# Performance work log

Measured on AMD Instinct MI355X. Metric: run time of the kernel, lower is better.

## Reference

```python
import jax, jax.numpy as jnp
import numpy as np

EPS = 1e-12  # matches torch F.normalize default eps


def setup_inputs() -> dict:
    key = jax.random.key(0)
    img_feats = jax.random.normal(key, (8192, 1024), dtype=jnp.float32)
    return {"img_feats": img_feats}


def reference(img_feats):
    # L2-normalize along feature dim (torch F.normalize: x / max(||x||, eps))
    norm = jnp.maximum(jnp.linalg.norm(img_feats, axis=-1, keepdims=True), EPS)
    feats_n = img_feats / norm                       # [N, D]
    sims = feats_n @ feats_n.T                        # [N, N] cosine similarities
    # mask self-similarity on the diagonal with -inf
    n = sims.shape[0]
    diag = jnp.arange(n)
    sims = sims.at[diag, diag].set(-jnp.inf)
    attn_weights = jax.nn.softmax(sims, axis=-1)      # [N, N]
    out = attn_weights @ img_feats                    # [N, D]
    return out, attn_weights
```

## Files before the change

kernel.cpp:

```cpp
#include <hip/hip_runtime.h>
#include <hip/hip_bf16.h>
#include <stdint.h>

#define NR 8192
#define ND 1024

typedef __attribute__((ext_vector_type(8))) short bf16x8;
typedef __attribute__((ext_vector_type(4))) float f32x4;
typedef __attribute__((ext_vector_type(4))) float fvec4;
typedef __attribute__((ext_vector_type(8))) unsigned short u16x8;

static __device__ __forceinline__ uint16_t f2bf(float f) {
  union { __hip_bfloat16 h; uint16_t u; } cv;
  cv.h = __float2bfloat16(f);
  return cv.u;
}
static __device__ __forceinline__ float bf2f(uint16_t u) {
  union { uint32_t i; float f; } cv;
  cv.i = ((uint32_t)u) << 16;
  return cv.f;
}

__global__ void k_norm(const float* __restrict__ X, uint16_t* __restrict__ Xn) {
  const int row = blockIdx.x;
  const int t = threadIdx.x;
  const float4 v = reinterpret_cast<const float4*>(X + (size_t)row * ND)[t];
  float ss = v.x * v.x + v.y * v.y + v.z * v.z + v.w * v.w;
#pragma unroll
  for (int m = 1; m < 64; m <<= 1) ss += __shfl_xor(ss, m, 64);
  __shared__ float sred[4];
  if ((t & 63) == 0) sred[t >> 6] = ss;
  __syncthreads();
  const float tot = sred[0] + sred[1] + sred[2] + sred[3];
  const float inv = 1.0f / fmaxf(sqrtf(tot), 1e-12f);
  ushort4 o;
  o.x = f2bf(v.x * inv); o.y = f2bf(v.y * inv);
  o.z = f2bf(v.z * inv); o.w = f2bf(v.w * inv);
  reinterpret_cast<ushort4*>(Xn + (size_t)row * ND)[t] = o;
}

__global__ void k_transpose(const float* __restrict__ X, uint16_t* __restrict__ XT) {
  __shared__ uint16_t tile[32][33];
  const int ntr = NR / 32;
  const int bx = blockIdx.x % ntr;
  const int by = blockIdx.x / ntr;
  const int r0 = bx * 32, d0 = by * 32;
  const int t = threadIdx.x;
  const int rr = t >> 3, cc = (t & 7) * 4;
  const float4 v = *reinterpret_cast<const float4*>(&X[(size_t)(r0 + rr) * ND + d0 + cc]);
  tile[cc + 0][rr] = f2bf(v.x);
  tile[cc + 1][rr] = f2bf(v.y);
  tile[cc + 2][rr] = f2bf(v.z);
  tile[cc + 3][rr] = f2bf(v.w);
  __syncthreads();
  ushort4 o;
  o.x = tile[rr][cc + 0]; o.y = tile[rr][cc + 1];
  o.z = tile[rr][cc + 2]; o.w = tile[rr][cc + 3];
  *reinterpret_cast<ushort4*>(&XT[(size_t)(d0 + rr) * NR + r0 + cc]) = o;
}

template <int MH, int NH>
static __device__ __forceinline__ void mfma16(f32x4 (&acc)[8][4],
                                              const bf16x8 (&a_)[4][2],
                                              const bf16x8 (&b_)[2][2]) {
  __builtin_amdgcn_s_setprio(1);
#pragma unroll
  for (int kk = 0; kk < 2; ++kk)
#pragma unroll
    for (int m4 = 0; m4 < 4; ++m4)
#pragma unroll
      for (int n2 = 0; n2 < 2; ++n2)
        acc[MH * 4 + m4][NH * 2 + n2] = __builtin_amdgcn_mfma_f32_16x16x32_bf16(
            a_[m4][kk], b_[n2][kk], acc[MH * 4 + m4][NH * 2 + n2], 0, 0, 0);
  __builtin_amdgcn_s_setprio(0);
}

#define BAR()    __builtin_amdgcn_s_barrier()
#define LGKM()   asm volatile("s_waitcnt lgkmcnt(0)" ::: "memory")
#define VMW4()   asm volatile("s_waitcnt vmcnt(4)" ::: "memory")
#define VMW0()   asm volatile("s_waitcnt vmcnt(0)" ::: "memory")
#define SCHED0() __builtin_amdgcn_sched_barrier(0)

template <int EPI, int NKT>
static __device__ __forceinline__ void gemm8_core(
    char* sm,
    const uint16_t* __restrict__ A, int lda,
    const uint16_t* __restrict__ B, int ldb,
    int row0, int col0,
    float* __restrict__ C, int ldc,
    uint16_t* __restrict__ Eo, float* __restrict__ partials, int rb, int cb,
    float* __restrict__ emitA, const float* __restrict__ invrs, int bx_emit) {
  const int tid = threadIdx.x;
  const int wid = tid >> 6;
  const int lane = tid & 63;
  const int wr = wid >> 2;
  const int wc = wid & 3;
  const int flane = lane & 15;
  const int qw = lane >> 4;
  const int rkey = flane & 7;
  const int rowb = flane * 128;

  const int colb = (((tid & 7) ^ ((tid >> 3) & 7)) * 16);
  const int r0s = tid >> 3;

  const char* const Abyte = (const char*)A + (size_t)row0 * lda * 2;
  const char* const Bbyte = (const char*)B + (size_t)col0 * ldb * 2;

  f32x4 acc[8][4] = {};
  bf16x8 a_[4][2], b_[2][2];

  float invr0 = 0, invr1 = 0, invr2 = 0, invr3 = 0;
  if constexpr (EPI == 1) {
    const int rb0 = tid >> 3;
    invr0 = invrs[row0 + rb0];
    invr1 = invrs[row0 + 64 + rb0];
    invr2 = invrs[row0 + 128 + rb0];
    invr3 = invrs[row0 + 192 + rb0];
  }

  auto stageH = [&](int d, int isB, int h, int t) {
    const char* gb = isB ? Bbyte : Abyte;
    const int ld2 = (isB ? ldb : lda) * 2;
    const char* g0 = gb + (size_t)(h * 128 + r0s) * ld2 + t * 128 + colb;
    const char* g1 = g0 + (size_t)64 * ld2;
    char* l0 = sm + d * 65536 + isB * 32768 + h * 16384 + (wid << 10);
    __builtin_amdgcn_global_load_lds((const __attribute__((address_space(1))) void*)g0,
                                     (__attribute__((address_space(3))) void*)l0, 16, 0, 0);
    __builtin_amdgcn_global_load_lds((const __attribute__((address_space(1))) void*)g1,
                                     (__attribute__((address_space(3))) void*)(l0 + 8192), 16, 0, 0);
  };
  auto rdA = [&](int d, int mhalf) {
#pragma unroll
    for (int m4 = 0; m4 < 4; ++m4)
#pragma unroll
      for (int kk = 0; kk < 2; ++kk) {
        const int chunk = (qw + kk * 4) ^ rkey;
        a_[m4][kk] = *(const bf16x8*)(sm + d * 65536 + wr * 16384 +
                                      (mhalf * 4 + m4) * 2048 + rowb + chunk * 16);
      }
  };
  auto rdB = [&](int d, int nhalf) {
#pragma unroll
    for (int n2 = 0; n2 < 2; ++n2)
#pragma unroll
      for (int kk = 0; kk < 2; ++kk) {
        const int chunk = (qw + kk * 4) ^ rkey;
        b_[n2][kk] = *(const bf16x8*)(sm + d * 65536 + 32768 + (wc >> 1) * 16384 +
                                      (wc & 1) * 8192 + (nhalf * 2 + n2) * 2048 +
                                      rowb + chunk * 16);
      }
  };
  auto emitT = [&](int d, int t) {
    const int c8 = tid & 7;
    const int rbase = tid >> 3;
#pragma unroll
    for (int p = 0; p < 4; ++p) {
      const int r = p * 64 + rbase;
      const u16x8 ev = *(const u16x8*)(sm + d * 65536 + ((r >> 7) * 16384) +
                                       (r & 127) * 128 + ((c8 ^ (r & 7)) << 4));
      const float inv = (p == 0) ? invr0 : (p == 1) ? invr1 : (p == 2) ? invr2 : invr3;
      fvec4 o0, o1;
      o0.x = bf2f(ev[0]) * inv; o0.y = bf2f(ev[1]) * inv;
      o0.z = bf2f(ev[2]) * inv; o0.w = bf2f(ev[3]) * inv;
      o1.x = bf2f(ev[4]) * inv; o1.y = bf2f(ev[5]) * inv;
      o1.z = bf2f(ev[6]) * inv; o1.w = bf2f(ev[7]) * inv;
      float* dst = emitA + (size_t)(row0 + r) * NR + t * 64 + c8 * 8;
      __builtin_nontemporal_store(o0, (fvec4*)dst);
      __builtin_nontemporal_store(o1, (fvec4*)(dst + 4));
    }
  };

  stageH(0, 0, 0, 0); stageH(0, 0, 1, 0); stageH(0, 1, 0, 0); stageH(0, 1, 1, 0);
  stageH(1, 0, 0, 1); stageH(1, 0, 1, 1);
  VMW4();
  BAR();

  const int niter = NKT / 2;
  for (int i = 0; i < niter; ++i) {
    const int t0 = 2 * i, t1 = t0 + 1;
    const bool s0 = (t0 + 2 < NKT), s1 = (t1 + 2 < NKT);
    const bool doEmit = (EPI == 1) && ((t0 >> 4) == bx_emit);
    rdA(0, 0); rdB(0, 0);
    stageH(1, 1, 0, t1); stageH(1, 1, 1, t1);
    BAR(); LGKM(); SCHED0(); mfma16<0, 0>(acc, a_, b_); BAR();
    rdB(0, 1);
    BAR(); LGKM(); SCHED0(); mfma16<0, 1>(acc, a_, b_); BAR();
    rdA(0, 1);
    BAR(); LGKM(); SCHED0(); mfma16<1, 1>(acc, a_, b_); BAR();
    if constexpr (EPI == 1) {
      if (doEmit) { emitT(0, t0); LGKM(); BAR(); }
    }
    rdB(0, 0);
    if (s0) { stageH(0, 0, 0, t0 + 2); stageH(0, 0, 1, t0 + 2); }
    BAR(); LGKM(); SCHED0(); mfma16<1, 0>(acc, a_, b_);
    if (s0) { VMW4(); } else { VMW0(); }
    BAR();
    rdA(1, 0); rdB(1, 0);
    if (s0) { stageH(0, 1, 0, t0 + 2); stageH(0, 1, 1, t0 + 2); }
    BAR(); LGKM(); SCHED0(); mfma16<0, 0>(acc, a_, b_); BAR();
    rdB(1, 1);
    BAR(); LGKM(); SCHED0(); mfma16<0, 1>(acc, a_, b_); BAR();
    rdA(1, 1);
    BAR(); LGKM(); SCHED0(); mfma16<1, 1>(acc, a_, b_); BAR();
    if constexpr (EPI == 1) {
      if (doEmit) { emitT(1, t1); LGKM(); BAR(); }
    }
    rdB(1, 0);
    if (s1) { stageH(1, 0, 0, t1 + 2); stageH(1, 0, 1, t1 + 2); }
    BAR(); LGKM(); SCHED0(); mfma16<1, 0>(acc, a_, b_);
    if (s1) { VMW4(); } else if (s0) { VMW0(); }
    BAR();
  }

  const int e0 = (lane >> 4) * 4;

  if constexpr (EPI == 0) {
    const bool diag = (rb == cb);
    float rp[8][4] = {};
    float rpT[4] = {};
#pragma unroll
    for (int m = 0; m < 8; ++m) {
      const int growb = row0 + wr * 128 + m * 16 + e0;
#pragma unroll
      for (int n = 0; n < 4; ++n) {
        const int gcol = col0 + wc * 64 + n * 16 + flane;
        ushort4 mpack;
#pragma unroll
        for (int e = 0; e < 4; ++e) {
          const int grow = growb + e;
          const float ev = (grow == gcol) ? 0.0f : __expf(acc[m][n][e]);
          const uint16_t eb = f2bf(ev);
          const float evr = bf2f(eb);
          Eo[(size_t)grow * NR + gcol] = eb;
          rp[m][e] += evr;
          rpT[n] += evr;
          ((uint16_t*)&mpack)[e] = eb;
        }
        if (!diag) {
          const int mr = wc * 64 + n * 16 + flane;
          const int mc = wr * 128 + m * 16 + e0;
          int byte = mr * 512 + mc * 2;
          byte ^= (mr & 7) << 4;
          *reinterpret_cast<ushort4*>(sm + byte) = mpack;
        }
      }
    }
#pragma unroll
    for (int msk = 1; msk <= 8; msk <<= 1)
#pragma unroll
      for (int m = 0; m < 8; ++m)
#pragma unroll
        for (int e = 0; e < 4; ++e) rp[m][e] += __shfl_xor(rp[m][e], msk, 64);
#pragma unroll
    for (int msk = 16; msk <= 32; msk <<= 1)
#pragma unroll
      for (int n = 0; n < 4; ++n) rpT[n] += __shfl_xor(rpT[n], msk, 64);

    __syncthreads();
    if (!diag) {
#pragma unroll
      for (int p = 0; p < 16; ++p) {
        const int mr = p * 16 + (tid >> 5);
        const int ch = tid & 31;
        int byte = mr * 512 + ch * 16;
        byte ^= (mr & 7) << 4;
        const u16x8 v = *reinterpret_cast<const u16x8*>(sm + byte);
        *reinterpret_cast<u16x8*>(&Eo[(size_t)(col0 + mr) * NR + row0 + ch * 8]) = v;
      }
    }
    __syncthreads();

    float* sRow = (float*)sm;
    float* sCol = (float*)(sm + 4096);
    if (flane == 0) {
#pragma unroll
      for (int m = 0; m < 8; ++m)
#pragma unroll
        for (int e = 0; e < 4; ++e)
          sRow[wc * 256 + wr * 128 + m * 16 + e0 + e] = rp[m][e];
    }
    if (lane < 16) {
#pragma unroll
      for (int n = 0; n < 4; ++n) sCol[wr * 256 + wc * 64 + n * 16 + lane] = rpT[n];
    }
    __syncthreads();
    if (tid < 256) {
      partials[(size_t)cb * NR + row0 + tid] =
          sRow[tid] + sRow[256 + tid] + sRow[512 + tid] + sRow[768 + tid];
      if (!diag)
        partials[(size_t)rb * NR + col0 + tid] = sCol[tid] + sCol[256 + tid];
    }
  } else {
#pragma unroll
    for (int m = 0; m < 8; ++m)
#pragma unroll
      for (int n = 0; n < 4; ++n)
#pragma unroll
        for (int e = 0; e < 4; ++e)
          C[(size_t)(row0 + wr * 128 + m * 16 + e0 + e) * ldc +
            col0 + wc * 64 + n * 16 + flane] = acc[m][n][e];
  }
}

__global__ __launch_bounds__(512, 2) void k_gemm_sym8(
    const uint16_t* __restrict__ Xn, uint16_t* __restrict__ E,
    float* __restrict__ partials) {
  extern __shared__ char smem[];
  const int nwg = gridDim.x;
  const int cpx = nwg >> 3;
  const int b = blockIdx.x;
  const int swz = (b & 7) * cpx + (b >> 3);
  int rem = swz, rb = 0;
  while (rem >= 32 - rb) { rem -= 32 - rb; ++rb; }
  const int cb = rb + rem;
  gemm8_core<0, 16>(smem, Xn, ND, Xn, ND, rb * 256, cb * 256,
                    nullptr, 0, E, partials, rb, cb, nullptr, nullptr, -1);
}

__global__ __launch_bounds__(512, 2) void k_gemm_pv8(
    const uint16_t* __restrict__ E, const uint16_t* __restrict__ XT,
    float* __restrict__ P, float* __restrict__ attn,
    const float* __restrict__ invrs) {
  extern __shared__ char smem[];
  const int b = blockIdx.x;
  const int swz = (b & 7) * 32 + (b >> 3);
  const int s = swz >> 7;
  const int t = swz & 127;
  const int by = t >> 2, bx = t & 3;
  gemm8_core<1, 64>(smem, E + (size_t)s * 4096, NR, XT + (size_t)s * 4096, NR,
                    by * 256, bx * 256, P + (size_t)s * NR * ND, ND,
                    nullptr, nullptr, 0, 0,
                    attn + (size_t)s * 4096, invrs, bx);
}

__global__ void k_rowsum(const float* __restrict__ partials, float* __restrict__ rowsum,
                         int ncb) {
  const int r = blockIdx.x * blockDim.x + threadIdx.x;
  float s = 0.0f;
  for (int cb = 0; cb < ncb; ++cb) s += partials[(size_t)cb * NR + r];
  rowsum[r] = 1.0f / s;
}

__global__ void k_fixup(const fvec4* __restrict__ P0, const fvec4* __restrict__ P1,
                        const float* __restrict__ rowsum, fvec4* __restrict__ out) {
  const size_t i = (size_t)blockIdx.x * blockDim.x + threadIdx.x;
  const int row = (int)(i >> 8);
  const float inv = rowsum[row];
  const fvec4 a = __builtin_nontemporal_load(&P0[i]);
  const fvec4 b = __builtin_nontemporal_load(&P1[i]);
  const fvec4 o = (a + b) * inv;
  __builtin_nontemporal_store(o, &out[i]);
}

extern "C" void kernel_launch(void* const* d_in, const int* in_sizes, int n_in,
                              void* d_out, int out_size, void* d_ws, size_t ws_size,
                              hipStream_t stream) {
  const float* X = (const float*)d_in[0];
  float* out = (float*)d_out;
  float* attn = out + (size_t)NR * ND;

  char* ws = (char*)d_ws;
  const size_t off_Xn   = 0;
  const size_t off_XT   = off_Xn + (size_t)NR * ND * 2;
  const size_t off_E    = off_XT + (size_t)ND * NR * 2;
  const size_t off_part = off_E + (size_t)NR * NR * 2;
  const size_t off_rs   = off_part + (size_t)64 * NR * 4;
  const size_t off_P    = off_rs + (size_t)NR * 4;
  const size_t needed   = off_P + (size_t)2 * NR * ND * 4;
  if (ws_size < needed) return;

  uint16_t* Xn  = (uint16_t*)(ws + off_Xn);
  uint16_t* XT  = (uint16_t*)(ws + off_XT);
  uint16_t* E   = (uint16_t*)(ws + off_E);
  float* partials = (float*)(ws + off_part);
  float* rowsum   = (float*)(ws + off_rs);
  float* P        = (float*)(ws + off_P);

  (void)hipFuncSetAttribute((const void*)k_gemm_sym8,
                            hipFuncAttributeMaxDynamicSharedMemorySize, 131072);
  (void)hipFuncSetAttribute((const void*)k_gemm_pv8,
                            hipFuncAttributeMaxDynamicSharedMemorySize, 131072);

  k_norm<<<NR, 256, 0, stream>>>(X, Xn);
  k_transpose<<<(NR / 32) * (ND / 32), 256, 0, stream>>>(X, XT);
  k_gemm_sym8<<<528, 512, 131072, stream>>>(Xn, E, partials);
  k_rowsum<<<NR / 256, 256, 0, stream>>>(partials, rowsum, 32);
  k_gemm_pv8<<<256, 512, 131072, stream>>>(E, XT, P, attn, rowsum);
  k_fixup<<<NR * ND / 4 / 256, 256, 0, stream>>>(
      (const fvec4*)P, (const fvec4*)(P + (size_t)NR * ND), rowsum, (fvec4*)out);
}
```

Before: 303.6 us.

## Rewrite PV GEMM with K=32 tiles and a four-stage load pipeline

```diff
diff --git a/kernel.cpp b/kernel.cpp
--- a/kernel.cpp
+++ b/kernel.cpp
@@ -9,6 +9,9 @@
 typedef __attribute__((ext_vector_type(4))) float f32x4;
 typedef __attribute__((ext_vector_type(4))) float fvec4;
 typedef __attribute__((ext_vector_type(8))) unsigned short u16x8;
+
+#define AS1 __attribute__((address_space(1)))
+#define AS3 __attribute__((address_space(3)))
 
 static __device__ __forceinline__ uint16_t f2bf(float f) {
   union { __hip_bfloat16 h; uint16_t u; } cv;
@@ -77,19 +80,16 @@
 
 #define BAR()    __builtin_amdgcn_s_barrier()
 #define LGKM()   asm volatile("s_waitcnt lgkmcnt(0)" ::: "memory")
+#define VMW12()  asm volatile("s_waitcnt vmcnt(12)" ::: "memory")
+#define VMW8()   asm volatile("s_waitcnt vmcnt(8)" ::: "memory")
 #define VMW4()   asm volatile("s_waitcnt vmcnt(4)" ::: "memory")
 #define VMW0()   asm volatile("s_waitcnt vmcnt(0)" ::: "memory")
 #define SCHED0() __builtin_amdgcn_sched_barrier(0)
 
-template <int EPI, int NKT>
-static __device__ __forceinline__ void gemm8_core(
-    char* sm,
-    const uint16_t* __restrict__ A, int lda,
-    const uint16_t* __restrict__ B, int ldb,
-    int row0, int col0,
-    float* __restrict__ C, int ldc,
-    uint16_t* __restrict__ Eo, float* __restrict__ partials, int rb, int cb,
-    float* __restrict__ emitA, const float* __restrict__ invrs, int bx_emit) {
+template <int NKT>
+static __device__ __forceinline__ void gemm_sym_core(
+    char* sm, const uint16_t* __restrict__ A, int lda, int row0, int col0,
+    uint16_t* __restrict__ Eo, float* __restrict__ partials, int rb, int cb) {
   const int tid = threadIdx.x;
   const int wid = tid >> 6;
   const int lane = tid & 63;
@@ -104,30 +104,19 @@
   const int r0s = tid >> 3;
 
   const char* const Abyte = (const char*)A + (size_t)row0 * lda * 2;
-  const char* const Bbyte = (const char*)B + (size_t)col0 * ldb * 2;
+  const char* const Bbyte = (const char*)A + (size_t)col0 * lda * 2;
 
   f32x4 acc[8][4] = {};
   bf16x8 a_[4][2], b_[2][2];
 
-  float invr0 = 0, invr1 = 0, invr2 = 0, invr3 = 0;
-  if constexpr (EPI == 1) {
-    const int rb0 = tid >> 3;
-    invr0 = invrs[row0 + rb0];
-    invr1 = invrs[row0 + 64 + rb0];
-    invr2 = invrs[row0 + 128 + rb0];
-    invr3 = invrs[row0 + 192 + rb0];
-  }
-
   auto stageH = [&](int d, int isB, int h, int t) {
     const char* gb = isB ? Bbyte : Abyte;
-    const int ld2 = (isB ? ldb : lda) * 2;
+    const int ld2 = lda * 2;
     const char* g0 = gb + (size_t)(h * 128 + r0s) * ld2 + t * 128 + colb;
     const char* g1 = g0 + (size_t)64 * ld2;
     char* l0 = sm + d * 65536 + isB * 32768 + h * 16384 + (wid << 10);
-    __builtin_amdgcn_global_load_lds((const __attribute__((address_space(1))) void*)g0,
-                                     (__attribute__((address_space(3))) void*)l0, 16, 0, 0);
-    __builtin_amdgcn_global_load_lds((const __attribute__((address_space(1))) void*)g1,
-                                     (__attribute__((address_space(3))) void*)(l0 + 8192), 16, 0, 0);
+    __builtin_amdgcn_global_load_lds((const AS1 void*)g0, (AS3 void*)l0, 16, 0, 0);
+    __builtin_amdgcn_global_load_lds((const AS1 void*)g1, (AS3 void*)(l0 + 8192), 16, 0, 0);
   };
   auto rdA = [&](int d, int mhalf) {
 #pragma unroll
@@ -150,25 +139,6 @@
                                       rowb + chunk * 16);
       }
   };
-  auto emitT = [&](int d, int t) {
-    const int c8 = tid & 7;
-    const int rbase = tid >> 3;
-#pragma unroll
-    for (int p = 0; p < 4; ++p) {
-      const int r = p * 64 + rbase;
-      const u16x8 ev = *(const u16x8*)(sm + d * 65536 + ((r >> 7) * 16384) +
-                                       (r & 127) * 128 + ((c8 ^ (r & 7)) << 4));
-      const float inv = (p == 0) ? invr0 : (p == 1) ? invr1 : (p == 2) ? invr2 : invr3;
-      fvec4 o0, o1;
-      o0.x = bf2f(ev[0]) * inv; o0.y = bf2f(ev[1]) * inv;
-      o0.z = bf2f(ev[2]) * inv; o0.w = bf2f(ev[3]) * inv;
-      o1.x = bf2f(ev[4]) * inv; o1.y = bf2f(ev[5]) * inv;
-      o1.z = bf2f(ev[6]) * inv; o1.w = bf2f(ev[7]) * inv;
-      float* dst = emitA + (size_t)(row0 + r) * NR + t * 64 + c8 * 8;
-      __builtin_nontemporal_store(o0, (fvec4*)dst);
-      __builtin_nontemporal_store(o1, (fvec4*)(dst + 4));
-    }
-  };
 
   stageH(0, 0, 0, 0); stageH(0, 0, 1, 0); stageH(0, 1, 0, 0); stageH(0, 1, 1, 0);
   stageH(1, 0, 0, 1); stageH(1, 0, 1, 1);
@@ -179,7 +149,6 @@
   for (int i = 0; i < niter; ++i) {
     const int t0 = 2 * i, t1 = t0 + 1;
     const bool s0 = (t0 + 2 < NKT), s1 = (t1 + 2 < NKT);
-    const bool doEmit = (EPI == 1) && ((t0 >> 4) == bx_emit);
     rdA(0, 0); rdB(0, 0);
     stageH(1, 1, 0, t1); stageH(1, 1, 1, t1);
     BAR(); LGKM(); SCHED0(); mfma16<0, 0>(acc, a_, b_); BAR();
@@ -187,9 +156,6 @@
     BAR(); LGKM(); SCHED0(); mfma16<0, 1>(acc, a_, b_); BAR();
     rdA(0, 1);
     BAR(); LGKM(); SCHED0(); mfma16<1, 1>(acc, a_, b_); BAR();
-    if constexpr (EPI == 1) {
-      if (doEmit) { emitT(0, t0); LGKM(); BAR(); }
-    }
     rdB(0, 0);
     if (s0) { stageH(0, 0, 0, t0 + 2); stageH(0, 0, 1, t0 + 2); }
     BAR(); LGKM(); SCHED0(); mfma16<1, 0>(acc, a_, b_);
@@ -202,9 +168,6 @@
     BAR(); LGKM(); SCHED0(); mfma16<0, 1>(acc, a_, b_); BAR();
     rdA(1, 1);
     BAR(); LGKM(); SCHED0(); mfma16<1, 1>(acc, a_, b_); BAR();
-    if constexpr (EPI == 1) {
-      if (doEmit) { emitT(1, t1); LGKM(); BAR(); }
-    }
     rdB(1, 0);
     if (s1) { stageH(1, 0, 0, t1 + 2); stageH(1, 0, 1, t1 + 2); }
     BAR(); LGKM(); SCHED0(); mfma16<1, 0>(acc, a_, b_);
@@ -213,92 +176,80 @@
   }
 
   const int e0 = (lane >> 4) * 4;
-
-  if constexpr (EPI == 0) {
-    const bool diag = (rb == cb);
-    float rp[8][4] = {};
-    float rpT[4] = {};
-#pragma unroll
-    for (int m = 0; m < 8; ++m) {
-      const int growb = row0 + wr * 128 + m * 16 + e0;
-#pragma unroll
-      for (int n = 0; n < 4; ++n) {
-        const int gcol = col0 + wc * 64 + n * 16 + flane;
-        ushort4 mpack;
-#pragma unroll
-        for (int e = 0; e < 4; ++e) {
-          const int grow = growb + e;
-          const float ev = (grow == gcol) ? 0.0f : __expf(acc[m][n][e]);
-          const uint16_t eb = f2bf(ev);
-          const float evr = bf2f(eb);
-          Eo[(size_t)grow * NR + gcol] = eb;
-          rp[m][e] += evr;
-          rpT[n] += evr;
-          ((uint16_t*)&mpack)[e] = eb;
-        }
-        if (!diag) {
-          const int mr = wc * 64 + n * 16 + flane;
-          const int mc = wr * 128 + m * 16 + e0;
-          int byte = mr * 512 + mc * 2;
-          byte ^= (mr & 7) << 4;
-          *reinterpret_cast<ushort4*>(sm + byte) = mpack;
-        }
+  const bool diag = (rb == cb);
+  float rp[8][4] = {};
+  float rpT[4] = {};
+#pragma unroll
+  for (int m = 0; m < 8; ++m) {
+    const int growb = row0 + wr * 128 + m * 16 + e0;
+#pragma unroll
+    for (int n = 0; n < 4; ++n) {
+      const int gcol = col0 + wc * 64 + n * 16 + flane;
+      ushort4 mpack;
+#pragma unroll
+      for (int e = 0; e < 4; ++e) {
+        const int grow = growb + e;
+        const float ev = (grow == gcol) ? 0.0f : __expf(acc[m][n][e]);
+        const uint16_t eb = f2bf(ev);
+        const float evr = bf2f(eb);
+        Eo[(size_t)grow * NR + gcol] = eb;
+        rp[m][e] += evr;
+        rpT[n] += evr;
+        ((uint16_t*)&mpack)[e] = eb;
+      }
+      if (!diag) {
+        const int mr = wc * 64 + n * 16 + flane;
+        const int mc = wr * 128 + m * 16 + e0;
+        int byte = mr * 512 + mc * 2;
+        byte ^= (mr & 7) << 4;
+        *reinterpret_cast<ushort4*>(sm + byte) = mpack;
       }
     }
-#pragma unroll
-    for (int msk = 1; msk <= 8; msk <<= 1)
-#pragma unroll
-      for (int m = 0; m < 8; ++m)
-#pragma unroll
-        for (int e = 0; e < 4; ++e) rp[m][e] += __shfl_xor(rp[m][e], msk, 64);
-#pragma unroll
-    for (int msk = 16; msk <= 32; msk <<= 1)
-#pragma unroll
-      for (int n = 0; n < 4; ++n) rpT[n] += __shfl_xor(rpT[n], msk, 64);
-
-    __syncthreads();
-    if (!diag) {
-#pragma unroll
-      for (int p = 0; p < 16; ++p) {
-        const int mr = p * 16 + (tid >> 5);
-        const int ch = tid & 31;
-        int byte = mr * 512 + ch * 16;
-        byte ^= (mr & 7) << 4;
-        const u16x8 v = *reinterpret_cast<const u16x8*>(sm + byte);
-        *reinterpret_cast<u16x8*>(&Eo[(size_t)(col0 + mr) * NR + row0 + ch * 8]) = v;
-      }
+  }
+#pragma unroll
+  for (int msk = 1; msk <= 8; msk <<= 1)
+#pragma unroll
+    for (int m = 0; m < 8; ++m)
+#pragma unroll
+      for (int e = 0; e < 4; ++e) rp[m][e] += __shfl_xor(rp[m][e], msk, 64);
+#pragma unroll
+  for (int msk = 16; msk <= 32; msk <<= 1)
+#pragma unroll
+    for (int n = 0; n < 4; ++n) rpT[n] += __shfl_xor(rpT[n], msk, 64);
+
+  __syncthreads();
+  if (!diag) {
+#pragma unroll
+    for (int p = 0; p < 16; ++p) {
+      const int mr = p * 16 + (tid >> 5);
+      const int ch = tid & 31;
+      int byte = mr * 512 + ch * 16;
+      byte ^= (mr & 7) << 4;
+      const u16x8 v = *reinterpret_cast<const u16x8*>(sm + byte);
+      *reinterpret_cast<u16x8*>(&Eo[(size_t)(col0 + mr) * NR + row0 + ch * 8]) = v;
     }
-    __syncthreads();
-
-    float* sRow = (float*)sm;
-    float* sCol = (float*)(sm + 4096);
-    if (flane == 0) {
-#pragma unroll
-      for (int m = 0; m < 8; ++m)
-#pragma unroll
-        for (int e = 0; e < 4; ++e)
-          sRow[wc * 256 + wr * 128 + m * 16 + e0 + e] = rp[m][e];
-    }
-    if (lane < 16) {
-#pragma unroll
-      for (int n = 0; n < 4; ++n) sCol[wr * 256 + wc * 64 + n * 16 + lane] = rpT[n];
-    }
-    __syncthreads();
-    if (tid < 256) {
-      partials[(size_t)cb * NR + row0 + tid] =
-          sRow[tid] + sRow[256 + tid] + sRow[512 + tid] + sRow[768 + tid];
-      if (!diag)
-        partials[(size_t)rb * NR + col0 + tid] = sCol[tid] + sCol[256 + tid];
-    }
-  } else {
+  }
+  __syncthreads();
+
+  float* sRow = (float*)sm;
+  float* sCol = (float*)(sm + 4096);
+  if (flane == 0) {
 #pragma unroll
     for (int m = 0; m < 8; ++m)
 #pragma unroll
-      for (int n = 0; n < 4; ++n)
-#pragma unroll
-        for (int e = 0; e < 4; ++e)
-          C[(size_t)(row0 + wr * 128 + m * 16 + e0 + e) * ldc +
-            col0 + wc * 64 + n * 16 + flane] = acc[m][n][e];
+      for (int e = 0; e < 4; ++e)
+        sRow[wc * 256 + wr * 128 + m * 16 + e0 + e] = rp[m][e];
+  }
+  if (lane < 16) {
+#pragma unroll
+    for (int n = 0; n < 4; ++n) sCol[wr * 256 + wc * 64 + n * 16 + lane] = rpT[n];
+  }
+  __syncthreads();
+  if (tid < 256) {
+    partials[(size_t)cb * NR + row0 + tid] =
+        sRow[tid] + sRow[256 + tid] + sRow[512 + tid] + sRow[768 + tid];
+    if (!diag)
+      partials[(size_t)rb * NR + col0 + tid] = sCol[tid] + sCol[256 + tid];
   }
 }
 
@@ -313,11 +264,10 @@
   int rem = swz, rb = 0;
   while (rem >= 32 - rb) { rem -= 32 - rb; ++rb; }
   const int cb = rb + rem;
-  gemm8_core<0, 16>(smem, Xn, ND, Xn, ND, rb * 256, cb * 256,
-                    nullptr, 0, E, partials, rb, cb, nullptr, nullptr, -1);
-}
-
-__global__ __launch_bounds__(512, 2) void k_gemm_pv8(
+  gemm_sym_core<16>(smem, Xn, ND, rb * 256, cb * 256, E, partials, rb, cb);
+}
+
+__global__ __launch_bounds__(512, 2) void k_pv32(
     const uint16_t* __restrict__ E, const uint16_t* __restrict__ XT,
     float* __restrict__ P, float* __restrict__ attn,
     const float* __restrict__ invrs) {
@@ -325,12 +275,106 @@
   const int b = blockIdx.x;
   const int swz = (b & 7) * 32 + (b >> 3);
   const int s = swz >> 7;
-  const int t = swz & 127;
-  const int by = t >> 2, bx = t & 3;
-  gemm8_core<1, 64>(smem, E + (size_t)s * 4096, NR, XT + (size_t)s * 4096, NR,
-                    by * 256, bx * 256, P + (size_t)s * NR * ND, ND,
-                    nullptr, nullptr, 0, 0,
-                    attn + (size_t)s * 4096, invrs, bx);
+  const int t4 = swz & 127;
+  const int by = t4 >> 2, bx = t4 & 3;
+  const int row0 = by * 256, col0 = bx * 256;
+
+  const int tid = threadIdx.x;
+  const int wid = tid >> 6;
+  const int lane = tid & 63;
+  const int wr = wid >> 2;
+  const int wc = wid & 3;
+  const int flane = lane & 15;
+  const int qw = lane >> 4;
+  const int keyL = (flane & 3) ^ ((flane >> 2) & 3);
+
+  const int skey = ((tid >> 2) & 3) ^ ((tid >> 4) & 3);
+  const int scol = ((tid & 3) ^ skey) << 4;
+  const int srow = tid >> 2;
+
+  const char* const Abyte = (const char*)(E + (size_t)s * 4096) + (size_t)row0 * NR * 2;
+  const char* const Bbyte = (const char*)(XT + (size_t)s * 4096) + (size_t)col0 * NR * 2;
+  float* const Pp = P + (size_t)s * NR * ND;
+  float* const emitA = attn + (size_t)s * 4096;
+
+  f32x4 acc[8][4] = {};
+
+  const float invr = invrs[row0 + (tid >> 1)];
+  const int keyE = ((tid >> 1) & 3) ^ ((tid >> 3) & 3);
+
+  auto stage = [&](int d, int t) {
+#pragma unroll
+    for (int isB = 0; isB < 2; ++isB)
+#pragma unroll
+      for (int h = 0; h < 2; ++h) {
+        const char* g = (isB ? Bbyte : Abyte) +
+                        (size_t)(h * 128 + srow) * (NR * 2) + t * 64 + scol;
+        char* l = smem + d * 32768 + isB * 16384 + h * 8192 + (wid << 10);
+        __builtin_amdgcn_global_load_lds((const AS1 void*)g, (AS3 void*)l, 16, 0, 0);
+      }
+  };
+
+  auto compute = [&](int d, int t, bool doEmit) {
+    bf16x8 a_[8], b_[4];
+#pragma unroll
+    for (int m = 0; m < 8; ++m) {
+      const int row = wr * 128 + m * 16 + flane;
+      a_[m] = *(const bf16x8*)(smem + d * 32768 + row * 64 + ((qw ^ keyL) << 4));
+    }
+#pragma unroll
+    for (int n = 0; n < 4; ++n) {
+      const int row = wc * 64 + n * 16 + flane;
+      b_[n] = *(const bf16x8*)(smem + d * 32768 + 16384 + row * 64 + ((qw ^ keyL) << 4));
+    }
+    LGKM(); SCHED0();
+    __builtin_amdgcn_s_setprio(1);
+#pragma unroll
+    for (int m = 0; m < 8; ++m)
+#pragma unroll
+      for (int n = 0; n < 4; ++n)
+        acc[m][n] = __builtin_amdgcn_mfma_f32_16x16x32_bf16(a_[m], b_[n], acc[m][n], 0, 0, 0);
+    __builtin_amdgcn_s_setprio(0);
+    if (doEmit) {
+      const int r = tid >> 1;
+#pragma unroll
+      for (int j = 0; j < 2; ++j) {
+        const int c = (tid & 1) * 2 + j;
+        const u16x8 ev = *(const u16x8*)(smem + d * 32768 + r * 64 + ((c ^ keyE) << 4));
+        fvec4 o0, o1;
+        o0.x = bf2f(ev[0]) * invr; o0.y = bf2f(ev[1]) * invr;
+        o0.z = bf2f(ev[2]) * invr; o0.w = bf2f(ev[3]) * invr;
+        o1.x = bf2f(ev[4]) * invr; o1.y = bf2f(ev[5]) * invr;
+        o1.z = bf2f(ev[6]) * invr; o1.w = bf2f(ev[7]) * invr;
+        float* dst = emitA + (size_t)(row0 + r) * NR + t * 32 + c * 8;
+        __builtin_nontemporal_store(o0, (fvec4*)dst);
+        __builtin_nontemporal_store(o1, (fvec4*)(dst + 4));
+      }
+      LGKM();
+    }
+  };
+
+  constexpr int NKT = 128;
+  stage(0, 0); stage(1, 1); stage(2, 2);
+  for (int t = 0; t < NKT - 3; ++t) {
+    stage((t + 3) & 3, t + 3);
+    VMW12();
+    BAR();
+    compute(t & 3, t, (t >> 5) == bx);
+    BAR();
+  }
+  VMW8();  BAR(); compute((NKT - 3) & 3, NKT - 3, ((NKT - 3) >> 5) == bx); BAR();
+  VMW4();  BAR(); compute((NKT - 2) & 3, NKT - 2, ((NKT - 2) >> 5) == bx); BAR();
+  VMW0();  BAR(); compute((NKT - 1) & 3, NKT - 1, ((NKT - 1) >> 5) == bx); BAR();
+
+  const int e0 = (lane >> 4) * 4;
+#pragma unroll
+  for (int m = 0; m < 8; ++m)
+#pragma unroll
+    for (int n = 0; n < 4; ++n)
+#pragma unroll
+      for (int e = 0; e < 4; ++e)
+        Pp[(size_t)(row0 + wr * 128 + m * 16 + e0 + e) * ND +
+           col0 + wc * 64 + n * 16 + flane] = acc[m][n][e];
 }
 
 __global__ void k_rowsum(const float* __restrict__ partials, float* __restrict__ rowsum,
@@ -378,14 +422,14 @@
 
   (void)hipFuncSetAttribute((const void*)k_gemm_sym8,
                             hipFuncAttributeMaxDynamicSharedMemorySize, 131072);
-  (void)hipFuncSetAttribute((const void*)k_gemm_pv8,
+  (void)hipFuncSetAttribute((const void*)k_pv32,
                             hipFuncAttributeMaxDynamicSharedMemorySize, 131072);
 
   k_norm<<<NR, 256, 0, stream>>>(X, Xn);
   k_transpose<<<(NR / 32) * (ND / 32), 256, 0, stream>>>(X, XT);
   k_gemm_sym8<<<528, 512, 131072, stream>>>(Xn, E, partials);
   k_rowsum<<<NR / 256, 256, 0, stream>>>(partials, rowsum, 32);
-  k_gemm_pv8<<<256, 512, 131072, stream>>>(E, XT, P, attn, rowsum);
+  k_pv32<<<256, 512, 131072, stream>>>(E, XT, P, attn, rowsum);
   k_fixup<<<NR * ND / 4 / 256, 256, 0, stream>>>(
       (const fvec4*)P, (const fvec4*)(P + (size_t)NR * ND), rowsum, (fvec4*)out);
 }
```

New measurement: 592.8 us. 1.95x slower.
